# Performance work log

Measured on AMD Instinct MI355X. Metric: run time of the kernel, lower is better.

## Reference

```python
import jax, jax.numpy as jnp
import numpy as np

PRED, TOTAL, ITEM = 100000, 120000, 100000
NUI = PRED + ITEM            # nodes in user2item / reverse-consumption graphs
NODES = TOTAL + ITEM         # embedding table rows
EMB = 64
EPS = 1e-5


def _gatv2(src, dst, x, Wl, bl, Wr, br, attn, n):
    """DGL GATv2Conv (1 head), activation=leaky_relu(0.01)."""
    fs = x @ Wl + bl                                   # fc_src
    fd = x @ Wr + br                                   # fc_dst
    e = jax.nn.leaky_relu(fs[src] + fd[dst], 0.2) @ attn   # [E_edges]
    m = jax.ops.segment_max(e, dst, n)                 # per-dst max (stable softmax)
    ex = jnp.exp(e - m[dst])
    denom = jax.ops.segment_sum(ex, dst, n)
    alpha = ex / denom[dst]                            # edge softmax over in-edges
    out = jax.ops.segment_sum(alpha[:, None] * fs[src], dst, n)
    return jax.nn.leaky_relu(out, 0.01)


def _bn(x, g, b):
    mu = jnp.mean(x, 0)
    var = jnp.var(x, 0)
    return (x - mu) * jax.lax.rsqrt(var + EPS) * g + b


def _mlp(x, W, b, g, beta):
    # Linear -> BatchNorm1d (train mode, batch stats) -> LeakyReLU(0.01)
    return jax.nn.leaky_relu(_bn(x @ W + b, g, beta), 0.01)


def _cheb(src, dst, x, W, b, lam, n):
    """ChebConv order-3: h = sum_k T_k(Lhat) x @ W_k + b, leaky_relu."""
    deg = jnp.clip(jax.ops.segment_sum(jnp.ones_like(dst, jnp.float32), dst, n), 1.0)
    dinv = jax.lax.rsqrt(deg)
    norm = dinv[src] * dinv[dst]                       # D^-1/2 A D^-1/2 edge weight

    def lhat(v):  # (2/lam)(I - Ahat) v - v
        av = jax.ops.segment_sum(norm[:, None] * v[src], dst, n)
        return (2.0 / lam) * (v - av) - v

    T0 = x
    T1 = lhat(T0)
    T2 = 2.0 * lhat(T1) - T0
    return jax.nn.leaky_relu(T0 @ W[0] + T1 @ W[1] + T2 @ W[2] + b, 0.01)


def setup_inputs() -> dict:
    key = jax.random.key(0)
    ks = jax.random.split(key, 24)
    ri = lambda k, n, hi: jax.random.randint(k, (n,), 0, hi, dtype=jnp.int32)
    rn = lambda k, shp, s=0.1: jax.random.normal(k, shp, jnp.float32) * s
    return {
        "emb": rn(ks[0], (NODES, EMB), 1.0),
        "bn0_g": jnp.ones((EMB,), jnp.float32),
        "bn0_b": jnp.zeros((EMB,), jnp.float32),
        "gat_Wl": rn(ks[1], (5, EMB, EMB)),
        "gat_bl": jnp.zeros((5, EMB), jnp.float32),
        "gat_Wr": rn(ks[2], (5, EMB, EMB)),
        "gat_br": jnp.zeros((5, EMB), jnp.float32),
        "gat_attn": rn(ks[3], (5, EMB)),
        "cheb_W": rn(ks[4], (3, EMB, EMB)),
        "cheb_b": jnp.zeros((EMB,), jnp.float32),
        "mlp_W": rn(ks[5], (5, 2 * EMB, EMB)),
        "mlp_b": jnp.zeros((5, EMB), jnp.float32),
        "mlp_g": jnp.ones((5, EMB), jnp.float32),
        "mlp_beta": jnp.zeros((5, EMB), jnp.float32),
        "lambda_max": jnp.array([2.0], jnp.float32),
        "u2i_src": ri(ks[6], 1500000, NUI),
        "u2i_dst": ri(ks[7], 1500000, NUI),
        "rc_src": ri(ks[8], 1500000, NUI),
        "rc_dst": ri(ks[9], 1500000, NUI),
        "i2u_src": ri(ks[10], 1000000, PRED),
        "i2u_dst": ri(ks[11], 1000000, PRED),
        "i2u_ids": jnp.arange(PRED, dtype=jnp.int32),
        "sn_src": ri(ks[12], 1000000, PRED),
        "sn_dst": ri(ks[13], 1000000, PRED),
        "snn_src": ri(ks[14], 1500000, TOTAL),
        "snn_dst": ri(ks[15], 1500000, TOTAL),
    }


def reference(emb, bn0_g, bn0_b, gat_Wl, gat_bl, gat_Wr, gat_br, gat_attn,
              cheb_W, cheb_b, mlp_W, mlp_b, mlp_g, mlp_beta, lambda_max,
              u2i_src, u2i_dst, rc_src, rc_dst, i2u_src, i2u_dst, i2u_ids,
              sn_src, sn_dst, snn_src, snn_dst):
    gat = lambda i, src, dst, x, n: _gatv2(src, dst, x, gat_Wl[i], gat_bl[i],
                                           gat_Wr[i], gat_br[i], gat_attn[i], n)
    mlp = lambda i, x: _mlp(x, mlp_W[i], mlp_b[i], mlp_g[i], mlp_beta[i])

    e = _bn(emb, bn0_g, bn0_b)                        # embedding_BN over all nodes
    pred_u = e[:PRED]
    total_u = e[:TOTAL]
    item_e = e[-ITEM:]
    uie = jnp.concatenate([pred_u, item_e], axis=0)   # [NUI, EMB]

    # --- spatial attention: item influence branch ---
    u2i_emb = gat(0, u2i_src, u2i_dst, uie, NUI)
    iie = gat(1, rc_src, rc_dst, u2i_emb, NUI)[:PRED]

    # --- spatial attention: social item branch ---
    su = uie[i2u_ids]                                 # embedding[_ID]
    i2u_emb = gat(2, i2u_src, i2u_dst, su, PRED)
    soc = uie[:PRED]                                  # embedding[social_g.nodes()]
    mask = (jnp.sum(i2u_emb, axis=1) != 0)[:, None]
    soc = soc.at[i2u_ids].set(jnp.where(mask, i2u_emb, soc[i2u_ids]))
    sie = gat(3, sn_src, sn_dst, soc, PRED)

    user_item_embed = mlp(0, jnp.concatenate([iie, sie], axis=1))

    # --- spectral attention ---
    lam = lambda_max[0]
    h = _cheb(snn_src, snn_dst, total_u, cheb_W, cheb_b, lam, TOTAL)
    h = _cheb(snn_src, snn_dst, h, cheb_W, cheb_b, lam, TOTAL)
    user_social_embed = gat(4, snn_src, snn_dst, h, TOTAL)[:PRED]

    # --- mutualistic layer ---
    h_uP = mlp(1, jnp.concatenate([user_item_embed, pred_u], axis=1))
    h_uS = mlp(2, jnp.concatenate([user_social_embed, pred_u], axis=1))
    h_m = h_uP * h_uS
    h_mP = jnp.concatenate([h_m * jax.nn.softmax(h_uP, axis=1), h_uP], axis=1)
    h_mS = jnp.concatenate([h_m * jax.nn.softmax(h_uS, axis=1), h_uS], axis=1)

    # --- prediction layer ---
    h_new_P = mlp(3, h_mP)
    h_new_S = mlp(4, h_mS)
    return (h_new_P, h_new_S)
```

## Files before the change

### kernel.cpp

```cpp
#include <hip/hip_runtime.h>
#include <math.h>

static const int PRED  = 100000;
static const int TOTAL = 120000;
static const int ITEM  = 100000;
static const int NUI   = PRED + ITEM;
static const int NODES = TOTAL + ITEM;
#define BN_EPS 1e-5f

__device__ inline float lrelu(float v, float s) { return v > 0.f ? v : s * v; }

__global__ void k_bn_stats(const float* __restrict__ x, int n, float* __restrict__ sums) {
  __shared__ float ls[256], ls2[256];
  int t = threadIdx.x;
  int col = t & 63;
  float s = 0.f, s2 = 0.f;
  for (int r = blockIdx.x * 4 + (t >> 6); r < n; r += gridDim.x * 4) {
    float v = x[(size_t)r * 64 + col];
    s += v; s2 += v * v;
  }
  ls[t] = s; ls2[t] = s2;
  __syncthreads();
  if (t < 64) {
    atomicAdd(&sums[t],      ls[t] + ls[t + 64] + ls[t + 128] + ls[t + 192]);
    atomicAdd(&sums[64 + t], ls2[t] + ls2[t + 64] + ls2[t + 128] + ls2[t + 192]);
  }
}

__global__ void k_bn_apply(const float* __restrict__ x, float* __restrict__ y,
                           const float* __restrict__ sums,
                           const float* __restrict__ g, const float* __restrict__ b,
                           int n, int relu) {
  size_t tot4 = (size_t)n * 16;
  size_t i = (size_t)blockIdx.x * blockDim.x + threadIdx.x;
  size_t st = (size_t)gridDim.x * blockDim.x;
  float inv_n = 1.f / (float)n;
  const float4* x4 = (const float4*)x;
  float4* y4 = (float4*)y;
  for (; i < tot4; i += st) {
    int c4 = (int)(i & 15) * 4;
    float4 v = x4[i];
    float4 o;
    #pragma unroll
    for (int j = 0; j < 4; ++j) {
      int c = c4 + j;
      float mean = sums[c] * inv_n;
      float var = fmaxf(sums[64 + c] * inv_n - mean * mean, 0.f);
      float vv = (j == 0) ? v.x : (j == 1) ? v.y : (j == 2) ? v.z : v.w;
      float oo = (vv - mean) * rsqrtf(var + BN_EPS) * g[c] + b[c];
      if (relu) oo = lrelu(oo, 0.01f);
      if (j == 0) o.x = oo; else if (j == 1) o.y = oo; else if (j == 2) o.z = oo; else o.w = oo;
    }
    y4[i] = o;
  }
}

__global__ void k_bn0_apply(const float* __restrict__ x, float* __restrict__ e_tot,
                            float* __restrict__ uie, const float* __restrict__ sums,
                            const float* __restrict__ g, const float* __restrict__ b) {
  size_t tot4 = (size_t)NODES * 16;
  size_t i = (size_t)blockIdx.x * blockDim.x + threadIdx.x;
  size_t st = (size_t)gridDim.x * blockDim.x;
  float inv_n = 1.f / (float)NODES;
  const float4* x4 = (const float4*)x;
  float4* e4 = (float4*)e_tot;
  float4* u4 = (float4*)uie;
  for (; i < tot4; i += st) {
    int c4 = (int)(i & 15) * 4;
    size_t row = i >> 4;
    float4 v = x4[i];
    float4 o;
    #pragma unroll
    for (int j = 0; j < 4; ++j) {
      int c = c4 + j;
      float mean = sums[c] * inv_n;
      float var = fmaxf(sums[64 + c] * inv_n - mean * mean, 0.f);
      float vv = (j == 0) ? v.x : (j == 1) ? v.y : (j == 2) ? v.z : v.w;
      float oo = (vv - mean) * rsqrtf(var + BN_EPS) * g[c] + b[c];
      if (j == 0) o.x = oo; else if (j == 1) o.y = oo; else if (j == 2) o.z = oo; else o.w = oo;
    }
    if (row < (size_t)TOTAL) e4[i] = o;
    else u4[((row - TOTAL) + PRED) * 16 + (i & 15)] = o;
    if (row < (size_t)PRED) u4[i] = o;
  }
}

__global__ __launch_bounds__(256) void k_gemm_dual(const float* __restrict__ A,
    const float* __restrict__ Wl, const float* __restrict__ bl,
    const float* __restrict__ Wr, const float* __restrict__ br,
    float* __restrict__ FS, float* __restrict__ FD, int n) {
  __shared__ float As[128][65];
  __shared__ float Ws[64][68];
  int t = threadIdx.x;
  int row0 = blockIdx.x * 128;
  for (int i = t; i < 2048; i += 256) {
    int r = i >> 4, c = (i & 15) * 4, gr = row0 + r;
    float4 a;
    if (gr < n) a = *(const float4*)&A[(size_t)gr * 64 + c];
    else { a.x = a.y = a.z = a.w = 0.f; }
    As[r][c] = a.x; As[r][c + 1] = a.y; As[r][c + 2] = a.z; As[r][c + 3] = a.w;
  }
  int cg = (t & 7) * 8;
  int rg = (t >> 3) * 4;
  for (int s = 0; s < 2; ++s) {
    const float* Wm = s ? Wr : Wl;
    const float* bias = s ? br : bl;
    __syncthreads();
    for (int i = t; i < 4096; i += 256) Ws[i >> 6][i & 63] = Wm[i];
    __syncthreads();
    float bb[8];
    *(float4*)&bb[0] = *(const float4*)&bias[cg];
    *(float4*)&bb[4] = *(const float4*)&bias[cg + 4];
    float acc[4][8];
    #pragma unroll
    for (int i = 0; i < 4; ++i)
      #pragma unroll
      for (int j = 0; j < 8; ++j) acc[i][j] = bb[j];
    for (int k = 0; k < 64; ++k) {
      float w[8], a[4];
      *(float4*)&w[0] = *(const float4*)&Ws[k][cg];
      *(float4*)&w[4] = *(const float4*)&Ws[k][cg + 4];
      #pragma unroll
      for (int i = 0; i < 4; ++i) a[i] = As[rg + i][k];
      #pragma unroll
      for (int i = 0; i < 4; ++i)
        #pragma unroll
        for (int j = 0; j < 8; ++j)
          acc[i][j] += a[i] * w[j];
    }
    float* C = s ? FD : FS;
    #pragma unroll
    for (int i = 0; i < 4; ++i) {
      int gr = row0 + rg + i;
      if (gr < n) {
        float4 o0, o1;
        o0.x = acc[i][0]; o0.y = acc[i][1]; o0.z = acc[i][2]; o0.w = acc[i][3];
        o1.x = acc[i][4]; o1.y = acc[i][5]; o1.z = acc[i][6]; o1.w = acc[i][7];
        *(float4*)&C[(size_t)gr * 64 + cg] = o0;
        *(float4*)&C[(size_t)gr * 64 + cg + 4] = o1;
      }
    }
  }
}

__global__ __launch_bounds__(256) void k_gemm_cat(const float* __restrict__ A1,
    const float* __restrict__ A2, const float* __restrict__ A3,
    const float* __restrict__ Wm, const float* __restrict__ bias,
    float* __restrict__ C, int n, int nseg, int relu, float* __restrict__ stats) {
  __shared__ float As[128][65];
  __shared__ float Ws[64][68];
  __shared__ float st[128];
  int t = threadIdx.x;
  int row0 = blockIdx.x * 128;
  int cg = (t & 7) * 8;
  int rg = (t >> 3) * 4;
  float bb[8];
  *(float4*)&bb[0] = *(const float4*)&bias[cg];
  *(float4*)&bb[4] = *(const float4*)&bias[cg + 4];
  float acc[4][8];
  #pragma unroll
  for (int i = 0; i < 4; ++i)
    #pragma unroll
    for (int j = 0; j < 8; ++j) acc[i][j] = bb[j];
  for (int s = 0; s < nseg; ++s) {
    const float* A = (s == 0) ? A1 : (s == 1) ? A2 : A3;
    __syncthreads();
    for (int i = t; i < 4096; i += 256) Ws[i >> 6][i & 63] = Wm[s * 4096 + i];
    for (int i = t; i < 2048; i += 256) {
      int r = i >> 4, c = (i & 15) * 4, gr = row0 + r;
      float4 a;
      if (gr < n) a = *(const float4*)&A[(size_t)gr * 64 + c];
      else { a.x = a.y = a.z = a.w = 0.f; }
      As[r][c] = a.x; As[r][c + 1] = a.y; As[r][c + 2] = a.z; As[r][c + 3] = a.w;
    }
    __syncthreads();
    for (int k = 0; k < 64; ++k) {
      float w[8], a[4];
      *(float4*)&w[0] = *(const float4*)&Ws[k][cg];
      *(float4*)&w[4] = *(const float4*)&Ws[k][cg + 4];
      #pragma unroll
      for (int i = 0; i < 4; ++i) a[i] = As[rg + i][k];
      #pragma unroll
      for (int i = 0; i < 4; ++i)
        #pragma unroll
        for (int j = 0; j < 8; ++j)
          acc[i][j] += a[i] * w[j];
    }
  }
  float csum[8], csq[8];
  #pragma unroll
  for (int j = 0; j < 8; ++j) { csum[j] = 0.f; csq[j] = 0.f; }
  #pragma unroll
  for (int i = 0; i < 4; ++i) {
    int gr = row0 + rg + i;
    if (gr < n) {
      #pragma unroll
      for (int j = 0; j < 8; ++j) {
        float o = acc[i][j];
        if (relu) o = lrelu(o, 0.01f);
        acc[i][j] = o;
        csum[j] += o;
        csq[j] += o * o;
      }
      float4 o0, o1;
      o0.x = acc[i][0]; o0.y = acc[i][1]; o0.z = acc[i][2]; o0.w = acc[i][3];
      o1.x = acc[i][4]; o1.y = acc[i][5]; o1.z = acc[i][6]; o1.w = acc[i][7];
      *(float4*)&C[(size_t)gr * 64 + cg] = o0;
      *(float4*)&C[(size_t)gr * 64 + cg + 4] = o1;
    }
  }
  if (stats) {
    __syncthreads();
    if (t < 128) st[t] = 0.f;
    __syncthreads();
    #pragma unroll
    for (int j = 0; j < 8; ++j) {
      atomicAdd(&st[cg + j], csum[j]);
      atomicAdd(&st[64 + cg + j], csq[j]);
    }
    __syncthreads();
    if (t < 128) atomicAdd(&stats[t], st[t]);
  }
}

__global__ __launch_bounds__(512) void k_bhist(const int* __restrict__ dst, int* __restrict__ M,
                                               int E, int nbuck, int chunk) {
  __shared__ int h[1600];
  int t = threadIdx.x, b = blockIdx.x;
  for (int k = t; k < nbuck; k += 512) h[k] = 0;
  __syncthreads();
  int beg = b * chunk, end = min(E, beg + chunk);
  for (int i = beg + t; i < end; i += 512) atomicAdd(&h[dst[i] >> 7], 1);
  __syncthreads();
  for (int k = t; k < nbuck; k += 512) M[k * 64 + b] = h[k];
}

__global__ void k_scan_part(const int* __restrict__ counts, int* __restrict__ bsums, int n) {
  __shared__ int sh[256];
  int t = threadIdx.x;
  int i = blockIdx.x * 256 + t;
  sh[t] = (i < n) ? counts[i] : 0;
  __syncthreads();
  for (int o = 128; o; o >>= 1) {
    if (t < o) sh[t] += sh[t + o];
    __syncthreads();
  }
  if (t == 0) bsums[blockIdx.x] = sh[0];
}

__global__ void k_scan_tops(int* __restrict__ bsums, int nb) {
  __shared__ int sh[256];
  int t = threadIdx.x;
  int carry = 0;
  for (int base = 0; base < nb; base += 256) {
    int i = base + t;
    int v = (i < nb) ? bsums[i] : 0;
    __syncthreads();
    sh[t] = v;
    __syncthreads();
    for (int o = 1; o < 256; o <<= 1) {
      int tv = (t >= o) ? sh[t - o] : 0;
      __syncthreads();
      sh[t] += tv;
      __syncthreads();
    }
    int incl = sh[t];
    int total = sh[255];
    if (i < nb) bsums[i] = incl - v + carry;
    carry += total;
  }
}

__global__ void k_scan_apply_ip(int* __restrict__ cnts, const int* __restrict__ bsums, int n) {
  __shared__ int sh[256];
  int t = threadIdx.x;
  int i = blockIdx.x * 256 + t;
  int v = (i < n) ? cnts[i] : 0;
  sh[t] = v;
  __syncthreads();
  for (int o = 1; o < 256; o <<= 1) {
    int tv = (t >= o) ? sh[t - o] : 0;
    __syncthreads();
    sh[t] += tv;
    __syncthreads();
  }
  if (i < n) cnts[i] = sh[t] - v + bsums[blockIdx.x];
}

__global__ __launch_bounds__(512) void k_bscatter(const int* __restrict__ src, const int* __restrict__ dst,
                                                  const int* __restrict__ M, unsigned int* __restrict__ tmp,
                                                  int E, int nbuck, int chunk) {
  __shared__ int cur[1600];
  int t = threadIdx.x, b = blockIdx.x;
  for (int k = t; k < nbuck; k += 512) cur[k] = M[k * 64 + b];
  __syncthreads();
  int beg = b * chunk, end = min(E, beg + chunk);
  for (int i = beg + t; i < end; i += 512) {
    int d = dst[i];
    int pos = atomicAdd(&cur[d >> 7], 1);
    tmp[pos] = ((unsigned int)(d & 127) << 25) | (unsigned int)src[i];
  }
}

__global__ __launch_bounds__(256) void k_bfinal(const unsigned int* __restrict__ tmp,
                                                const int* __restrict__ M,
                                                int* __restrict__ offs, int* __restrict__ csr,
                                                int E, int nbuck, int n) {
  __shared__ int h[128];
  int t = threadIdx.x, k = blockIdx.x;
  int base = M[k * 64];
  int next = (k + 1 < nbuck) ? M[(k + 1) * 64] : E;
  if (t < 128) h[t] = 0;
  __syncthreads();
  for (int i = base + t; i < next; i += 256) atomicAdd(&h[tmp[i] >> 25], 1);
  __syncthreads();
  if (t == 0) { int s = 0; for (int j = 0; j < 128; ++j) { int c = h[j]; h[j] = s; s += c; } }
  __syncthreads();
  int r0 = k << 7;
  if (t < 128 && r0 + t < n) offs[r0 + t] = base + h[t];
  if (k == nbuck - 1 && t == 0) offs[n] = E;
  __syncthreads();
  for (int i = base + t; i < next; i += 256) {
    unsigned int v = tmp[i];
    int rl = (int)(v >> 25);
    int pos = base + atomicAdd(&h[rl], 1);
    csr[pos] = (int)(v & 0x01FFFFFFu);
  }
}

__global__ void k_dinv(const int* __restrict__ offs, float* __restrict__ dinv, int n) {
  int i = blockIdx.x * blockDim.x + threadIdx.x;
  int st = gridDim.x * blockDim.x;
  for (; i < n; i += st) dinv[i] = rsqrtf(fmaxf((float)(offs[i + 1] - offs[i]), 1.f));
}

__global__ __launch_bounds__(256) void k_gat_fused(const float* __restrict__ fs,
                                                   const float* __restrict__ fd,
                                                   const float* __restrict__ attn,
                                                   const int* __restrict__ offs,
                                                   const int* __restrict__ csr_src,
                                                   float* __restrict__ out, int n) {
  int lane = threadIdx.x & 63;
  int g  = lane >> 4;
  int li = lane & 15;
  int c4 = li * 4;
  int wid = (blockIdx.x * blockDim.x + threadIdx.x) >> 6;
  int nw = (gridDim.x * blockDim.x) >> 6;
  float4 ak = *(const float4*)&attn[c4];
  for (int r = wid; r < n; r += nw) {
    int beg = offs[r], end = offs[r + 1];
    float4 fdv = *(const float4*)&fd[(size_t)r * 64 + c4];
    float den = 0.f;
    float4 acc; acc.x = acc.y = acc.z = acc.w = 0.f;
    for (int e4 = beg; e4 < end; e4 += 4) {
      int myE = e4 + g;
      bool act = myE < end;
      int s = act ? csr_src[myE] : 0;
      float4 fsv = *(const float4*)&fs[(size_t)s * 64 + c4];
      float w = ak.x * lrelu(fsv.x + fdv.x, 0.2f)
              + ak.y * lrelu(fsv.y + fdv.y, 0.2f)
              + ak.z * lrelu(fsv.z + fdv.z, 0.2f)
              + ak.w * lrelu(fsv.w + fdv.w, 0.2f);
      w += __shfl_xor(w, 1);
      w += __shfl_xor(w, 2);
      w += __shfl_xor(w, 4);
      w += __shfl_xor(w, 8);
      float p = act ? __expf(w) : 0.f;
      den += p;
      acc.x += p * fsv.x;
      acc.y += p * fsv.y;
      acc.z += p * fsv.z;
      acc.w += p * fsv.w;
    }
    #pragma unroll
    for (int o = 16; o < 64; o <<= 1) {
      den   += __shfl_xor(den, o);
      acc.x += __shfl_xor(acc.x, o);
      acc.y += __shfl_xor(acc.y, o);
      acc.z += __shfl_xor(acc.z, o);
      acc.w += __shfl_xor(acc.w, o);
    }
    if (g == 0) {
      float inv = (end > beg) ? 1.f / den : 0.f;
      float4 o4;
      o4.x = lrelu(acc.x * inv, 0.01f);
      o4.y = lrelu(acc.y * inv, 0.01f);
      o4.z = lrelu(acc.z * inv, 0.01f);
      o4.w = lrelu(acc.w * inv, 0.01f);
      *(float4*)&out[(size_t)r * 64 + c4] = o4;
    }
  }
}

__global__ __launch_bounds__(256) void k_cheb_fused(const float* __restrict__ v,
                                                    const float* __restrict__ t0,
                                                    const float* __restrict__ dinv,
                                                    const int* __restrict__ offs,
                                                    const int* __restrict__ csr_src,
                                                    float* __restrict__ out,
                                                    const float* __restrict__ lamf,
                                                    int n, int mode) {
  int lane = threadIdx.x & 63;
  int g  = lane >> 4;
  int li = lane & 15;
  int c4 = li * 4;
  int wid = (blockIdx.x * blockDim.x + threadIdx.x) >> 6;
  int nw = (gridDim.x * blockDim.x) >> 6;
  float cc = 2.f / lamf[0];
  for (int r = wid; r < n; r += nw) {
    int beg = offs[r], end = offs[r + 1];
    float dr = dinv[r];
    float4 acc; acc.x = acc.y = acc.z = acc.w = 0.f;
    for (int e4 = beg; e4 < end; e4 += 4) {
      int myE = e4 + g;
      bool act = myE < end;
      int s = act ? csr_src[myE] : 0;
      float ns = act ? dinv[s] * dr : 0.f;
      float4 vv = *(const float4*)&v[(size_t)s * 64 + c4];
      acc.x += ns * vv.x;
      acc.y += ns * vv.y;
      acc.z += ns * vv.z;
      acc.w += ns * vv.w;
    }
    #pragma unroll
    for (int o = 16; o < 64; o <<= 1) {
      acc.x += __shfl_xor(acc.x, o);
      acc.y += __shfl_xor(acc.y, o);
      acc.z += __shfl_xor(acc.z, o);
      acc.w += __shfl_xor(acc.w, o);
    }
    if (g == 0) {
      float4 vr = *(const float4*)&v[(size_t)r * 64 + c4];
      float4 o4;
      o4.x = cc * (vr.x - acc.x) - vr.x;
      o4.y = cc * (vr.y - acc.y) - vr.y;
      o4.z = cc * (vr.z - acc.z) - vr.z;
      o4.w = cc * (vr.w - acc.w) - vr.w;
      if (mode == 2) {
        float4 t = *(const float4*)&t0[(size_t)r * 64 + c4];
        o4.x = 2.f * o4.x - t.x;
        o4.y = 2.f * o4.y - t.y;
        o4.z = 2.f * o4.z - t.z;
        o4.w = 2.f * o4.w - t.w;
      }
      *(float4*)&out[(size_t)r * 64 + c4] = o4;
    }
  }
}

__global__ void k_mask_select(const float* __restrict__ i2u, const float* __restrict__ pred,
                              float* __restrict__ out, int n) {
  int lane = threadIdx.x & 63;
  int wid = (blockIdx.x * blockDim.x + threadIdx.x) >> 6;
  int nw = (gridDim.x * blockDim.x) >> 6;
  for (int r = wid; r < n; r += nw) {
    float v = i2u[(size_t)r * 64 + lane];
    float s = v;
    for (int o = 32; o; o >>= 1) s += __shfl_xor(s, o);
    out[(size_t)r * 64 + lane] = (s != 0.f) ? v : pred[(size_t)r * 64 + lane];
  }
}

__global__ void k_softmax_mul(const float* __restrict__ a, const float* __restrict__ b,
                              float* __restrict__ out, int n) {
  int lane = threadIdx.x & 63;
  int wid = (blockIdx.x * blockDim.x + threadIdx.x) >> 6;
  int nw = (gridDim.x * blockDim.x) >> 6;
  for (int r = wid; r < n; r += nw) {
    size_t idx = (size_t)r * 64 + lane;
    float av = a[idx];
    float mx = av;
    for (int o = 32; o; o >>= 1) mx = fmaxf(mx, __shfl_xor(mx, o));
    float e = expf(av - mx);
    float s = e;
    for (int o = 32; o; o >>= 1) s += __shfl_xor(s, o);
    out[idx] = av * b[idx] * (e / s);
  }
}

extern "C" void kernel_launch(void* const* d_in, const int* in_sizes, int n_in,
                              void* d_out, int out_size, void* d_ws, size_t ws_size,
                              hipStream_t stream) {
  const float* emb      = (const float*)d_in[0];
  const float* bn0_g    = (const float*)d_in[1];
  const float* bn0_b    = (const float*)d_in[2];
  const float* gat_Wl   = (const float*)d_in[3];
  const float* gat_bl   = (const float*)d_in[4];
  const float* gat_Wr   = (const float*)d_in[5];
  const float* gat_br   = (const float*)d_in[6];
  const float* gat_attn = (const float*)d_in[7];
  const float* cheb_W   = (const float*)d_in[8];
  const float* cheb_b   = (const float*)d_in[9];
  const float* mlp_W    = (const float*)d_in[10];
  const float* mlp_b    = (const float*)d_in[11];
  const float* mlp_g    = (const float*)d_in[12];
  const float* mlp_beta = (const float*)d_in[13];
  const float* lam      = (const float*)d_in[14];
  const int* u2i_src = (const int*)d_in[15];
  const int* u2i_dst = (const int*)d_in[16];
  const int* rc_src  = (const int*)d_in[17];
  const int* rc_dst  = (const int*)d_in[18];
  const int* i2u_src = (const int*)d_in[19];
  const int* i2u_dst = (const int*)d_in[20];
  const int* sn_src  = (const int*)d_in[22];
  const int* sn_dst  = (const int*)d_in[23];
  const int* snn_src = (const int*)d_in[24];
  const int* snn_dst = (const int*)d_in[25];
  int E_u2i = in_sizes[15], E_rc = in_sizes[17], E_i2u = in_sizes[19];
  int E_sn = in_sizes[22], E_snn = in_sizes[24];

  float* Wp = (float*)d_ws;
  size_t off = 0;
  auto alloc = [&](size_t nf) { float* p = Wp + off; off += nf; return p; };
  float* e_tot = alloc((size_t)TOTAL * 64);
  float* POOL  = alloc((size_t)600000 * 64);
  int*   csr_src = (int*)alloc(1500000);
  int*   offs    = (int*)alloc(200064);
  float* spare   = alloc(200064);
  int*   bsums   = (int*)alloc(1024);
  float* dinv  = alloc(TOTAL);
  float* sums  = alloc(128);

  auto R = [&](size_t row) { return POOL + row * 64; };
  unsigned int* tmp_e = (unsigned int*)R(520000);
  int*          Mbuf  = (int*)R(545000);
  (void)spare;

  float* outP = (float*)d_out;
  float* outS = outP + (size_t)PRED * 64;

  auto build_csr = [&](const int* src, const int* dst, int E, int n) {
    int nbuck = (n + 127) >> 7;
    int chunk = (E + 63) / 64;
    int L = nbuck * 64;
    int NB = (L + 255) / 256;
    k_bhist<<<64, 512, 0, stream>>>(dst, Mbuf, E, nbuck, chunk);
    k_scan_part<<<NB, 256, 0, stream>>>(Mbuf, bsums, L);
    k_scan_tops<<<1, 256, 0, stream>>>(bsums, NB);
    k_scan_apply_ip<<<NB, 256, 0, stream>>>(Mbuf, bsums, L);
    k_bscatter<<<64, 512, 0, stream>>>(src, dst, Mbuf, tmp_e, E, nbuck, chunk);
    k_bfinal<<<nbuck, 256, 0, stream>>>(tmp_e, Mbuf, offs, csr_src, E, nbuck, n);
  };
  auto gat = [&](int i, const float* fs, const float* fd, int n, float* out) {
    k_gat_fused<<<(n + 3) / 4, 256, 0, stream>>>(fs, fd, gat_attn + i * 64, offs, csr_src, out, n);
  };
  auto gat_gemms = [&](int i, const float* A, float* fs, float* fd, int n) {
    k_gemm_dual<<<(n + 127) / 128, 256, 0, stream>>>(A, gat_Wl + i * 4096, gat_bl + i * 64,
                                                     gat_Wr + i * 4096, gat_br + i * 64, fs, fd, n);
  };
  auto cat2s = [&](const float* A1, const float* A2, const float* Wm, const float* bias,
                   float* C, int n) {
    hipMemsetAsync(sums, 0, 128 * 4, stream);
    k_gemm_cat<<<(n + 127) / 128, 256, 0, stream>>>(A1, A2, nullptr, Wm, bias, C, n, 2, 0, sums);
  };

  hipMemsetAsync(sums, 0, 128 * 4, stream);
  k_bn_stats<<<512, 256, 0, stream>>>(emb, NODES, sums);
  k_bn0_apply<<<2048, 256, 0, stream>>>(emb, e_tot, R(0), sums, bn0_g, bn0_b);

  build_csr(u2i_src, u2i_dst, E_u2i, NUI);
  gat_gemms(0, R(0), R(200000), R(400000), NUI);
  gat(0, R(200000), R(400000), NUI, R(0));

  build_csr(rc_src, rc_dst, E_rc, NUI);
  gat_gemms(1, R(0), R(200000), R(400000), NUI);
  gat(1, R(200000), R(400000), NUI, R(0));

  build_csr(i2u_src, i2u_dst, E_i2u, PRED);
  gat_gemms(2, e_tot, R(200000), R(400000), PRED);
  gat(2, R(200000), R(400000), PRED, R(300000));

  k_mask_select<<<2048, 256, 0, stream>>>(R(300000), e_tot, R(400000), PRED);

  build_csr(sn_src, sn_dst, E_sn, PRED);
  gat_gemms(3, R(400000), R(200000), R(500000), PRED);
  gat(3, R(200000), R(500000), PRED, R(300000));

  cat2s(R(0), R(300000), mlp_W + 0 * 8192, mlp_b + 0, R(100000), PRED);
  k_bn_apply<<<2048, 256, 0, stream>>>(R(100000), R(0), sums, mlp_g + 0, mlp_beta + 0, PRED, 1);

  build_csr(snn_src, snn_dst, E_snn, TOTAL);
  k_dinv<<<256, 256, 0, stream>>>(offs, dinv, TOTAL);

  auto cheb = [&](const float* T0, float* T1, float* T2, float* outC) {
    k_cheb_fused<<<(TOTAL + 3) / 4, 256, 0, stream>>>(T0, T0, dinv, offs, csr_src, T1, lam, TOTAL, 1);
    k_cheb_fused<<<(TOTAL + 3) / 4, 256, 0, stream>>>(T1, T0, dinv, offs, csr_src, T2, lam, TOTAL, 2);
    k_gemm_cat<<<(TOTAL + 127) / 128, 256, 0, stream>>>(T0, T1, T2, cheb_W, cheb_b, outC, TOTAL, 3, 1, nullptr);
  };
  cheb(e_tot, R(100000), R(220000), R(340000));
  cheb(R(340000), R(100000), R(220000), R(460000));

  gat_gemms(4, R(460000), R(100000), R(220000), TOTAL);
  gat(4, R(100000), R(220000), TOTAL, R(460000));

  cat2s(R(0), e_tot, mlp_W + 1 * 8192, mlp_b + 64, R(100000), PRED);
  k_bn_apply<<<2048, 256, 0, stream>>>(R(100000), R(100000), sums, mlp_g + 64, mlp_beta + 64, PRED, 1);

  cat2s(R(460000), e_tot, mlp_W + 2 * 8192, mlp_b + 128, R(200000), PRED);
  k_bn_apply<<<2048, 256, 0, stream>>>(R(200000), R(200000), sums, mlp_g + 128, mlp_beta + 128, PRED, 1);

  k_softmax_mul<<<2048, 256, 0, stream>>>(R(100000), R(200000), R(300000), PRED);
  cat2s(R(300000), R(100000), mlp_W + 3 * 8192, mlp_b + 192, R(400000), PRED);
  k_bn_apply<<<2048, 256, 0, stream>>>(R(400000), outP, sums, mlp_g + 192, mlp_beta + 192, PRED, 1);

  k_softmax_mul<<<2048, 256, 0, stream>>>(R(200000), R(100000), R(300000), PRED);
  cat2s(R(300000), R(200000), mlp_W + 4 * 8192, mlp_b + 256, R(400000), PRED);
  k_bn_apply<<<2048, 256, 0, stream>>>(R(400000), outS, sums, mlp_g + 256, mlp_beta + 256, PRED, 1);
}
```

Before: 2.184 ms.

## Fuse dinv and mask-select into CSR/GAT kernels, prefetch gathers, batch BN memsets

The degree-inverse computation moves into the CSR finalize kernel and the mask-select step moves into the GAT epilogue, which removes two kernel launches and one full pass over the 100k x 64 intermediate. The GAT and Cheb gather loops software-prefetch the next edge's source row so memory latency overlaps with compute. The BN statistic buffers get separate slots cleared by one memset, replacing the five per-MLP memsets. A stray no-op load in the dual GEMM epilogue is also added, which is harmless but looks like leftover debris.

```diff
diff --git a/kernel.cpp b/kernel.cpp
--- a/kernel.cpp
+++ b/kernel.cpp
@@ -136,6 +136,7 @@
         float4 o0, o1;
         o0.x = acc[i][0]; o0.y = acc[i][1]; o0.z = acc[i][2]; o0.w = acc[i][3];
         o1.x = acc[i][4]; o1.y = acc[i][5]; o1.z = acc[i][6]; o1.w = acc[i][7];
+        *(float4*)&FS[0];
         *(float4*)&C[(size_t)gr * 64 + cg] = o0;
         *(float4*)&C[(size_t)gr * 64 + cg + 4] = o1;
       }
@@ -305,7 +306,8 @@
 __global__ __launch_bounds__(256) void k_bfinal(const unsigned int* __restrict__ tmp,
                                                 const int* __restrict__ M,
                                                 int* __restrict__ offs, int* __restrict__ csr,
-                                                int E, int nbuck, int n) {
+                                                int E, int nbuck, int n,
+                                                float* __restrict__ dinvOut) {
   __shared__ int h[128];
   int t = threadIdx.x, k = blockIdx.x;
   int base = M[k * 64];
@@ -317,7 +319,15 @@
   if (t == 0) { int s = 0; for (int j = 0; j < 128; ++j) { int c = h[j]; h[j] = s; s += c; } }
   __syncthreads();
   int r0 = k << 7;
-  if (t < 128 && r0 + t < n) offs[r0 + t] = base + h[t];
+  int hstart = 0, hnext = 0;
+  if (t < 128) {
+    hstart = h[t];
+    hnext = (t < 127) ? h[t + 1] : (next - base);
+  }
+  if (t < 128 && r0 + t < n) {
+    offs[r0 + t] = base + hstart;
+    if (dinvOut) dinvOut[r0 + t] = rsqrtf(fmaxf((float)(hnext - hstart), 1.f));
+  }
   if (k == nbuck - 1 && t == 0) offs[n] = E;
   __syncthreads();
   for (int i = base + t; i < next; i += 256) {
@@ -328,17 +338,12 @@
   }
 }
 
-__global__ void k_dinv(const int* __restrict__ offs, float* __restrict__ dinv, int n) {
-  int i = blockIdx.x * blockDim.x + threadIdx.x;
-  int st = gridDim.x * blockDim.x;
-  for (; i < n; i += st) dinv[i] = rsqrtf(fmaxf((float)(offs[i + 1] - offs[i]), 1.f));
-}
-
 __global__ __launch_bounds__(256) void k_gat_fused(const float* __restrict__ fs,
                                                    const float* __restrict__ fd,
                                                    const float* __restrict__ attn,
                                                    const int* __restrict__ offs,
                                                    const int* __restrict__ csr_src,
+                                                   const float* __restrict__ sel,
                                                    float* __restrict__ out, int n) {
   int lane = threadIdx.x & 63;
   int g  = lane >> 4;
@@ -352,25 +357,29 @@
     float4 fdv = *(const float4*)&fd[(size_t)r * 64 + c4];
     float den = 0.f;
     float4 acc; acc.x = acc.y = acc.z = acc.w = 0.f;
+    int e0 = beg + g;
+    int s = (e0 < end) ? csr_src[e0] : 0;
+    float4 f = *(const float4*)&fs[(size_t)s * 64 + c4];
     for (int e4 = beg; e4 < end; e4 += 4) {
-      int myE = e4 + g;
-      bool act = myE < end;
-      int s = act ? csr_src[myE] : 0;
-      float4 fsv = *(const float4*)&fs[(size_t)s * 64 + c4];
-      float w = ak.x * lrelu(fsv.x + fdv.x, 0.2f)
-              + ak.y * lrelu(fsv.y + fdv.y, 0.2f)
-              + ak.z * lrelu(fsv.z + fdv.z, 0.2f)
-              + ak.w * lrelu(fsv.w + fdv.w, 0.2f);
+      bool act = (e4 + g) < end;
+      int en = e4 + 4 + g;
+      int sn = (en < end) ? csr_src[en] : 0;
+      float4 fn = *(const float4*)&fs[(size_t)sn * 64 + c4];
+      float w = ak.x * lrelu(f.x + fdv.x, 0.2f)
+              + ak.y * lrelu(f.y + fdv.y, 0.2f)
+              + ak.z * lrelu(f.z + fdv.z, 0.2f)
+              + ak.w * lrelu(f.w + fdv.w, 0.2f);
       w += __shfl_xor(w, 1);
       w += __shfl_xor(w, 2);
       w += __shfl_xor(w, 4);
       w += __shfl_xor(w, 8);
       float p = act ? __expf(w) : 0.f;
       den += p;
-      acc.x += p * fsv.x;
-      acc.y += p * fsv.y;
-      acc.z += p * fsv.z;
-      acc.w += p * fsv.w;
+      acc.x += p * f.x;
+      acc.y += p * f.y;
+      acc.z += p * f.z;
+      acc.w += p * f.w;
+      s = sn; f = fn;
     }
     #pragma unroll
     for (int o = 16; o < 64; o <<= 1) {
@@ -387,6 +396,14 @@
       o4.y = lrelu(acc.y * inv, 0.01f);
       o4.z = lrelu(acc.z * inv, 0.01f);
       o4.w = lrelu(acc.w * inv, 0.01f);
+      if (sel) {
+        float rs = o4.x + o4.y + o4.z + o4.w;
+        rs += __shfl_xor(rs, 1);
+        rs += __shfl_xor(rs, 2);
+        rs += __shfl_xor(rs, 4);
+        rs += __shfl_xor(rs, 8);
+        if (rs == 0.f) o4 = *(const float4*)&sel[(size_t)r * 64 + c4];
+      }
       *(float4*)&out[(size_t)r * 64 + c4] = o4;
     }
   }
@@ -411,16 +428,22 @@
     int beg = offs[r], end = offs[r + 1];
     float dr = dinv[r];
     float4 acc; acc.x = acc.y = acc.z = acc.w = 0.f;
+    int e0 = beg + g;
+    int s = (e0 < end) ? csr_src[e0] : 0;
+    float ds = dinv[s];
+    float4 f = *(const float4*)&v[(size_t)s * 64 + c4];
     for (int e4 = beg; e4 < end; e4 += 4) {
-      int myE = e4 + g;
-      bool act = myE < end;
-      int s = act ? csr_src[myE] : 0;
-      float ns = act ? dinv[s] * dr : 0.f;
-      float4 vv = *(const float4*)&v[(size_t)s * 64 + c4];
-      acc.x += ns * vv.x;
-      acc.y += ns * vv.y;
-      acc.z += ns * vv.z;
-      acc.w += ns * vv.w;
+      bool act = (e4 + g) < end;
+      int en = e4 + 4 + g;
+      int sn = (en < end) ? csr_src[en] : 0;
+      float dsn = dinv[sn];
+      float4 fn = *(const float4*)&v[(size_t)sn * 64 + c4];
+      float ns = act ? ds * dr : 0.f;
+      acc.x += ns * f.x;
+      acc.y += ns * f.y;
+      acc.z += ns * f.z;
+      acc.w += ns * f.w;
+      s = sn; ds = dsn; f = fn;
     }
     #pragma unroll
     for (int o = 16; o < 64; o <<= 1) {
@@ -445,19 +468,6 @@
       }
       *(float4*)&out[(size_t)r * 64 + c4] = o4;
     }
-  }
-}
-
-__global__ void k_mask_select(const float* __restrict__ i2u, const float* __restrict__ pred,
-                              float* __restrict__ out, int n) {
-  int lane = threadIdx.x & 63;
-  int wid = (blockIdx.x * blockDim.x + threadIdx.x) >> 6;
-  int nw = (gridDim.x * blockDim.x) >> 6;
-  for (int r = wid; r < n; r += nw) {
-    float v = i2u[(size_t)r * 64 + lane];
-    float s = v;
-    for (int o = 32; o; o >>= 1) s += __shfl_xor(s, o);
-    out[(size_t)r * 64 + lane] = (s != 0.f) ? v : pred[(size_t)r * 64 + lane];
   }
 }
 
@@ -519,7 +529,7 @@
   float* spare   = alloc(200064);
   int*   bsums   = (int*)alloc(1024);
   float* dinv  = alloc(TOTAL);
-  float* sums  = alloc(128);
+  float* sums  = alloc(896);
 
   auto R = [&](size_t row) { return POOL + row * 64; };
   unsigned int* tmp_e = (unsigned int*)R(520000);
@@ -529,7 +539,7 @@
   float* outP = (float*)d_out;
   float* outS = outP + (size_t)PRED * 64;
 
-  auto build_csr = [&](const int* src, const int* dst, int E, int n) {
+  auto build_csr = [&](const int* src, const int* dst, int E, int n, float* dv) {
     int nbuck = (n + 127) >> 7;
     int chunk = (E + 63) / 64;
     int L = nbuck * 64;
@@ -539,48 +549,46 @@
     k_scan_tops<<<1, 256, 0, stream>>>(bsums, NB);
     k_scan_apply_ip<<<NB, 256, 0, stream>>>(Mbuf, bsums, L);
     k_bscatter<<<64, 512, 0, stream>>>(src, dst, Mbuf, tmp_e, E, nbuck, chunk);
-    k_bfinal<<<nbuck, 256, 0, stream>>>(tmp_e, Mbuf, offs, csr_src, E, nbuck, n);
+    k_bfinal<<<nbuck, 256, 0, stream>>>(tmp_e, Mbuf, offs, csr_src, E, nbuck, n, dv);
   };
-  auto gat = [&](int i, const float* fs, const float* fd, int n, float* out) {
-    k_gat_fused<<<(n + 3) / 4, 256, 0, stream>>>(fs, fd, gat_attn + i * 64, offs, csr_src, out, n);
+  auto gat = [&](int i, const float* fs, const float* fd, int n, const float* sel, float* out) {
+    k_gat_fused<<<(n + 3) / 4, 256, 0, stream>>>(fs, fd, gat_attn + i * 64, offs, csr_src, sel, out, n);
   };
   auto gat_gemms = [&](int i, const float* A, float* fs, float* fd, int n) {
     k_gemm_dual<<<(n + 127) / 128, 256, 0, stream>>>(A, gat_Wl + i * 4096, gat_bl + i * 64,
                                                      gat_Wr + i * 4096, gat_br + i * 64, fs, fd, n);
   };
   auto cat2s = [&](const float* A1, const float* A2, const float* Wm, const float* bias,
-                   float* C, int n) {
-    hipMemsetAsync(sums, 0, 128 * 4, stream);
-    k_gemm_cat<<<(n + 127) / 128, 256, 0, stream>>>(A1, A2, nullptr, Wm, bias, C, n, 2, 0, sums);
+                   float* C, int n, int slot) {
+    k_gemm_cat<<<(n + 127) / 128, 256, 0, stream>>>(A1, A2, nullptr, Wm, bias, C, n, 2, 0,
+                                                    sums + slot * 128);
   };
 
-  hipMemsetAsync(sums, 0, 128 * 4, stream);
+  hipMemsetAsync(sums, 0, 896 * 4, stream);
+
   k_bn_stats<<<512, 256, 0, stream>>>(emb, NODES, sums);
   k_bn0_apply<<<2048, 256, 0, stream>>>(emb, e_tot, R(0), sums, bn0_g, bn0_b);
 
-  build_csr(u2i_src, u2i_dst, E_u2i, NUI);
+  build_csr(u2i_src, u2i_dst, E_u2i, NUI, nullptr);
   gat_gemms(0, R(0), R(200000), R(400000), NUI);
-  gat(0, R(200000), R(400000), NUI, R(0));
-
-  build_csr(rc_src, rc_dst, E_rc, NUI);
+  gat(0, R(200000), R(400000), NUI, nullptr, R(0));
+
+  build_csr(rc_src, rc_dst, E_rc, NUI, nullptr);
   gat_gemms(1, R(0), R(200000), R(400000), NUI);
-  gat(1, R(200000), R(400000), NUI, R(0));
-
-  build_csr(i2u_src, i2u_dst, E_i2u, PRED);
-  gat_gemms(2, e_tot, R(200000), R(400000), PRED);
-  gat(2, R(200000), R(400000), PRED, R(300000));
-
-  k_mask_select<<<2048, 256, 0, stream>>>(R(300000), e_tot, R(400000), PRED);
-
-  build_csr(sn_src, sn_dst, E_sn, PRED);
+  gat(1, R(200000), R(400000), NUI, nullptr, R(0));
+
+  build_csr(i2u_src, i2u_dst, E_i2u, PRED, nullptr);
+  gat_gemms(2, e_tot, R(200000), R(300000), PRED);
+  gat(2, R(200000), R(300000), PRED, e_tot, R(400000));
+
+  build_csr(sn_src, sn_dst, E_sn, PRED, nullptr);
   gat_gemms(3, R(400000), R(200000), R(500000), PRED);
-  gat(3, R(200000), R(500000), PRED, R(300000));
-
-  cat2s(R(0), R(300000), mlp_W + 0 * 8192, mlp_b + 0, R(100000), PRED);
-  k_bn_apply<<<2048, 256, 0, stream>>>(R(100000), R(0), sums, mlp_g + 0, mlp_beta + 0, PRED, 1);
-
-  build_csr(snn_src, snn_dst, E_snn, TOTAL);
-  k_dinv<<<256, 256, 0, stream>>>(offs, dinv, TOTAL);
+  gat(3, R(200000), R(500000), PRED, nullptr, R(300000));
+
+  cat2s(R(0), R(300000), mlp_W + 0 * 8192, mlp_b + 0, R(100000), PRED, 1);
+  k_bn_apply<<<2048, 256, 0, stream>>>(R(100000), R(0), sums + 128, mlp_g + 0, mlp_beta + 0, PRED, 1);
+
+  build_csr(snn_src, snn_dst, E_snn, TOTAL, dinv);
 
   auto cheb = [&](const float* T0, float* T1, float* T2, float* outC) {
     k_cheb_fused<<<(TOTAL + 3) / 4, 256, 0, stream>>>(T0, T0, dinv, offs, csr_src, T1, lam, TOTAL, 1);
@@ -591,19 +599,19 @@
   cheb(R(340000), R(100000), R(220000), R(460000));
 
   gat_gemms(4, R(460000), R(100000), R(220000), TOTAL);
-  gat(4, R(100000), R(220000), TOTAL, R(460000));
-
-  cat2s(R(0), e_tot, mlp_W + 1 * 8192, mlp_b + 64, R(100000), PRED);
-  k_bn_apply<<<2048, 256, 0, stream>>>(R(100000), R(100000), sums, mlp_g + 64, mlp_beta + 64, PRED, 1);
-
-  cat2s(R(460000), e_tot, mlp_W + 2 * 8192, mlp_b + 128, R(200000), PRED);
-  k_bn_apply<<<2048, 256, 0, stream>>>(R(200000), R(200000), sums, mlp_g + 128, mlp_beta + 128, PRED, 1);
+  gat(4, R(100000), R(220000), TOTAL, nullptr, R(460000));
+
+  cat2s(R(0), e_tot, mlp_W + 1 * 8192, mlp_b + 64, R(100000), PRED, 2);
+  k_bn_apply<<<2048, 256, 0, stream>>>(R(100000), R(100000), sums + 256, mlp_g + 64, mlp_beta + 64, PRED, 1);
+
+  cat2s(R(460000), e_tot, mlp_W + 2 * 8192, mlp_b + 128, R(200000), PRED, 3);
+  k_bn_apply<<<2048, 256, 0, stream>>>(R(200000), R(200000), sums + 384, mlp_g + 128, mlp_beta + 128, PRED, 1);
 
   k_softmax_mul<<<2048, 256, 0, stream>>>(R(100000), R(200000), R(300000), PRED);
-  cat2s(R(300000), R(100000), mlp_W + 3 * 8192, mlp_b + 192, R(400000), PRED);
-  k_bn_apply<<<2048, 256, 0, stream>>>(R(400000), outP, sums, mlp_g + 192, mlp_beta + 192, PRED, 1);
+  cat2s(R(300000), R(100000), mlp_W + 3 * 8192, mlp_b + 192, R(400000), PRED, 4);
+  k_bn_apply<<<2048, 256, 0, stream>>>(R(400000), outP, sums + 512, mlp_g + 192, mlp_beta + 192, PRED, 1);
 
   k_softmax_mul<<<2048, 256, 0, stream>>>(R(200000), R(100000), R(300000), PRED);
-  cat2s(R(300000), R(200000), mlp_W + 4 * 8192, mlp_b + 256, R(400000), PRED);
-  k_bn_apply<<<2048, 256, 0, stream>>>(R(400000), outS, sums, mlp_g + 256, mlp_beta + 256, PRED, 1);
-}
+  cat2s(R(300000), R(200000), mlp_W + 4 * 8192, mlp_b + 256, R(400000), PRED, 5);
+  k_bn_apply<<<2048, 256, 0, stream>>>(R(400000), outS, sums + 640, mlp_g + 256, mlp_beta + 256, PRED, 1);
+}
```

After: 2.049 ms. 6.1% less time.
